# Optimization experiments

Measured on AMD Instinct MI355X. Metric: run time of the kernel, lower is better.

The kernel has to match this reference:

```python
import jax, jax.numpy as jnp
import numpy as np

NUM_HEADS = 8

def setup_inputs() -> dict:
    key = jax.random.key(0)
    ks = jax.random.split(key, 7)
    B, C, H, W = 8, 256, 32, 32
    scale = 1.0 / np.sqrt(C)
    return {
        "x": jax.random.normal(ks[0], (B, C, H, W), dtype=jnp.float32),
        "Wq": jax.random.normal(ks[1], (C, C), dtype=jnp.float32) * scale,
        "bq": jax.random.normal(ks[2], (C,), dtype=jnp.float32) * 0.01,
        "Wk": jax.random.normal(ks[3], (C, C), dtype=jnp.float32) * scale,
        "bk": jax.random.normal(ks[4], (C,), dtype=jnp.float32) * 0.01,
        "Wv": jax.random.normal(ks[5], (C, C), dtype=jnp.float32) * scale,
        "bv": jax.random.normal(ks[6], (C,), dtype=jnp.float32) * 0.01,
        "gamma": jnp.zeros((1,), dtype=jnp.float32),
    }

def reference(x, Wq, bq, Wk, bk, Wv, bv, gamma):
    B, C, H, W = x.shape
    nh = NUM_HEADS
    hd = C // nh
    N = H * W
    xf = x.reshape(B, C, N)  # flatten spatial dims; 1x1 conv == channel matmul

    def proj(Wt, bt):
        y = jnp.einsum('oc,bcn->bon', Wt, xf) + bt[None, :, None]
        return y.reshape(B, nh, hd, N)

    q = proj(Wq, bq)  # [B, h, d, N]
    k = proj(Wk, bk)
    v = proj(Wv, bv)

    # scores: q^T k over head_dim -> [B, h, N, N]
    scores = jnp.einsum('bhdn,bhdm->bhnm', q, k) / (hd ** 0.5)
    attn = jax.nn.softmax(scores, axis=-1)
    # out = attn @ v^T, arranged back to [B, h, d, N]
    out = jnp.einsum('bhnm,bhdm->bhdn', attn, v).reshape(B, C, H, W)
    return gamma * out + x
```

## Files before the change

kernel.cpp:

```cpp
#include <hip/hip_runtime.h>

typedef float f4 __attribute__((ext_vector_type(4)));
typedef __bf16 bf16x8 __attribute__((ext_vector_type(8)));
typedef unsigned short us4 __attribute__((ext_vector_type(4)));
typedef unsigned short us8 __attribute__((ext_vector_type(8)));
typedef unsigned int u2 __attribute__((ext_vector_type(2)));

#define NB 8
#define NC 256
#define NSP 1024
#define NH 8
#define HD 32
#define QSCALE_L2E 0.25506065038580317f

__device__ __forceinline__ unsigned short f2bf(float f) {
  unsigned u = __builtin_bit_cast(unsigned, f);
  u += 0x7FFFu + ((u >> 16) & 1u);
  return (unsigned short)(u >> 16);
}

__device__ __forceinline__ unsigned pkbf(float a, float b) {
  unsigned r;
  asm("v_cvt_pk_bf16_f32 %0, %1, %2" : "=v"(r) : "v"(a), "v"(b));
  return r;
}

__global__ __launch_bounds__(256) void prep_kernel(
    const float* __restrict__ x, const float* __restrict__ Wq,
    const float* __restrict__ Wk, const float* __restrict__ Wv,
    unsigned short* __restrict__ xT, unsigned short* __restrict__ wbf) {
  const int t = threadIdx.x;
  if (blockIdx.z == 8) {
    const int flat = (blockIdx.y * 16 + blockIdx.x) * 256 + t;
    const float* Ws[3] = {Wq, Wk, Wv};
#pragma unroll
    for (int p = 0; p < 3; ++p) {
      const f4 v = reinterpret_cast<const f4*>(Ws[p])[flat];
      us4 o;
#pragma unroll
      for (int j = 0; j < 4; ++j) o[j] = f2bf(v[j]);
      reinterpret_cast<us4*>(wbf + (size_t)p * 65536)[flat] = o;
    }
    return;
  }
  const int b = blockIdx.z;
  const int nt = blockIdx.x * 64, ct = blockIdx.y * 64;
  __shared__ float xs[64][72];
  const int cl = t >> 4, nl = (t & 15) * 4;
#pragma unroll
  for (int r = 0; r < 4; ++r) {
    const f4 v = *reinterpret_cast<const f4*>(
        &x[((size_t)(b * NC + ct + cl + r * 16)) * NSP + nt + nl]);
    *reinterpret_cast<f4*>(&xs[cl + r * 16][nl]) = v;
  }
  __syncthreads();
  const int n = t >> 2, cq = (t & 3) * 16;
  us8 o0, o1;
#pragma unroll
  for (int i = 0; i < 8; ++i) o0[i] = f2bf(xs[cq + i][n]);
#pragma unroll
  for (int i = 0; i < 8; ++i) o1[i] = f2bf(xs[cq + 8 + i][n]);
  const size_t base = ((size_t)(b * NSP + nt + n)) * NC + ct + cq;
  *reinterpret_cast<us8*>(&xT[base]) = o0;
  *reinterpret_cast<us8*>(&xT[base + 8]) = o1;
}

__global__ __launch_bounds__(256) void proj_qkv_kernel(
    const unsigned short* __restrict__ wbf, const float* __restrict__ bq,
    const float* __restrict__ bk, const float* __restrict__ bv,
    const unsigned short* __restrict__ xT, unsigned short* __restrict__ dq,
    unsigned short* __restrict__ dk, unsigned short* __restrict__ dv) {
  const int id = blockIdx.x;
  const int xcd = id & 7, rem = id >> 3;
  const int z = rem % 3;
  const int p = xcd + 8 * (rem / 3);
  const int ntile = (p & 15) * 64;
  const int b = p >> 4;

  const unsigned short* W = wbf + (size_t)z * 65536;
  const float* bias = (z == 0) ? bq : (z == 1) ? bk : bv;
  unsigned short* dst = (z == 0) ? dq : (z == 1) ? dk : dv;

  const int t = threadIdx.x, wid = t >> 6, lane = t & 63;
  const int lr = lane & 15, lg = lane >> 4;
  const int o0 = wid * 64;
  const size_t xbase = ((size_t)b * NSP + ntile) * NC;

  f4 acc[4][4] = {};
  for (int kk = 0; kk < NC; kk += 32) {
    bf16x8 wf[4], xf[4];
#pragma unroll
    for (int i = 0; i < 4; ++i)
      wf[i] = *reinterpret_cast<const bf16x8*>(
          &W[(size_t)(o0 + i * 16 + lr) * NC + kk + lg * 8]);
#pragma unroll
    for (int j = 0; j < 4; ++j)
      xf[j] = *reinterpret_cast<const bf16x8*>(
          &xT[xbase + (size_t)(j * 16 + lr) * NC + kk + lg * 8]);
    if (z != 2) {
#pragma unroll
      for (int i = 0; i < 4; ++i)
#pragma unroll
        for (int j = 0; j < 4; ++j)
          acc[i][j] = __builtin_amdgcn_mfma_f32_16x16x32_bf16(
              wf[i], xf[j], acc[i][j], 0, 0, 0);
    } else {
#pragma unroll
      for (int i = 0; i < 4; ++i)
#pragma unroll
        for (int j = 0; j < 4; ++j)
          acc[i][j] = __builtin_amdgcn_mfma_f32_16x16x32_bf16(
              xf[i], wf[j], acc[i][j], 0, 0, 0);
    }
  }

  if (z != 2) {
    const float scale = (z == 0) ? QSCALE_L2E : 1.0f;
#pragma unroll
    for (int i = 0; i < 4; ++i) {
      const int o = o0 + i * 16 + lg * 4;
      const f4 bvv = *reinterpret_cast<const f4*>(&bias[o]);
      const int h = o >> 5, d = o & 31;
#pragma unroll
      for (int j = 0; j < 4; ++j) {
        const int n = ntile + j * 16 + lr;
        us4 pk;
#pragma unroll
        for (int r = 0; r < 4; ++r) pk[r] = f2bf((acc[i][j][r] + bvv[r]) * scale);
        *reinterpret_cast<us4*>(
            &dst[(((size_t)b * NH + h) * NSP + n) * HD + d]) = pk;
      }
    }
  } else {
#pragma unroll
    for (int j = 0; j < 4; ++j) {
      const int o = o0 + j * 16 + lr;
      const float bo = bias[o];
      const int h = o >> 5, d = o & 31;
#pragma unroll
      for (int i = 0; i < 4; ++i) {
        const int n = ntile + i * 16 + lg * 4;
        us4 pk;
#pragma unroll
        for (int r = 0; r < 4; ++r) pk[r] = f2bf(acc[i][j][r] + bo);
        *reinterpret_cast<us4*>(
            &dst[(((size_t)b * NH + h) * HD + d) * NSP + n]) = pk;
      }
    }
  }
}

__global__ __launch_bounds__(256) void attn_kernel(
    const unsigned short* __restrict__ qs, const unsigned short* __restrict__ ks,
    const unsigned short* __restrict__ vt, const float* __restrict__ x,
    const float* __restrict__ gamma, float* __restrict__ out) {
  const int id = blockIdx.x;
  const int xcd = id & 7, slot = id >> 3;
  const int bh = xcd * 8 + (slot & 7);
  const int qt = slot >> 3;
  const int t = threadIdx.x, wid = t >> 6, lane = t & 63;
  const int lr = lane & 15, lg = lane >> 4;
  const int qbase = qt * 128 + wid * 32;

  __shared__ unsigned short plds[4][32][72];
  unsigned short* pw = &plds[wid][0][0];

  const size_t kvbase = (size_t)bh * (NSP * HD);
  bf16x8 qa[2];
#pragma unroll
  for (int qf = 0; qf < 2; ++qf)
    qa[qf] = *reinterpret_cast<const bf16x8*>(
        &qs[kvbase + (size_t)(qbase + qf * 16 + lr) * HD + lg * 8]);

  const unsigned short* kp = ks + kvbase;
  const unsigned short* vp = vt + kvbase;

  f4 acc[2][2] = {};
  float ls[2] = {0.f, 0.f};

  bf16x8 kb[4], vb[4];
#pragma unroll
  for (int kf = 0; kf < 4; ++kf)
    kb[kf] = *reinterpret_cast<const bf16x8*>(
        &kp[(size_t)(kf * 16 + lr) * HD + lg * 8]);
#pragma unroll
  for (int i = 0; i < 4; ++i) {
    const int sk = i >> 1, c = i & 1;
    vb[i] = *reinterpret_cast<const bf16x8*>(
        &vp[(size_t)(c * 16 + lr) * NSP + sk * 32 + lg * 8]);
  }

  for (int kt = 0; kt < NSP; kt += 64) {
    bf16x8 ck[4], cv[4];
#pragma unroll
    for (int i = 0; i < 4; ++i) { ck[i] = kb[i]; cv[i] = vb[i]; }
    const int nk = (kt + 64) & (NSP - 1);
#pragma unroll
    for (int kf = 0; kf < 4; ++kf)
      kb[kf] = *reinterpret_cast<const bf16x8*>(
          &kp[(size_t)(nk + kf * 16 + lr) * HD + lg * 8]);
#pragma unroll
    for (int i = 0; i < 4; ++i) {
      const int sk = i >> 1, c = i & 1;
      vb[i] = *reinterpret_cast<const bf16x8*>(
          &vp[(size_t)(c * 16 + lr) * NSP + nk + sk * 32 + lg * 8]);
    }

    const f4 z4 = {0.f, 0.f, 0.f, 0.f};
    f4 st[2][4];
#pragma unroll
    for (int qf = 0; qf < 2; ++qf)
#pragma unroll
      for (int kf = 0; kf < 4; ++kf)
        st[qf][kf] =
            __builtin_amdgcn_mfma_f32_16x16x32_bf16(ck[kf], qa[qf], z4, 0, 0, 0);

#pragma unroll
    for (int qf = 0; qf < 2; ++qf) {
      float lsum = 0.f;
#pragma unroll
      for (int kf = 0; kf < 4; ++kf) {
        f4 e;
#pragma unroll
        for (int r = 0; r < 4; ++r) e[r] = __builtin_exp2f(st[qf][kf][r]);
        lsum += (e[0] + e[1]) + (e[2] + e[3]);
        u2 wv = {pkbf(e[0], e[1]), pkbf(e[2], e[3])};
        *reinterpret_cast<u2*>(&pw[(qf * 16 + lr) * 72 + kf * 16 + lg * 4]) = wv;
      }
      ls[qf] += lsum;
    }

    bf16x8 pa[2][2];
#pragma unroll
    for (int sk = 0; sk < 2; ++sk)
#pragma unroll
      for (int qf = 0; qf < 2; ++qf)
        pa[sk][qf] = *reinterpret_cast<const bf16x8*>(
            &pw[(qf * 16 + lr) * 72 + sk * 32 + lg * 8]);

#pragma unroll
    for (int sk = 0; sk < 2; ++sk)
#pragma unroll
      for (int qf = 0; qf < 2; ++qf)
#pragma unroll
        for (int c = 0; c < 2; ++c)
          acc[qf][c] = __builtin_amdgcn_mfma_f32_16x16x32_bf16(
              pa[sk][qf], cv[sk * 2 + c], acc[qf][c], 0, 0, 0);
  }

#pragma unroll
  for (int qf = 0; qf < 2; ++qf) {
    ls[qf] += __shfl_xor(ls[qf], 16);
    ls[qf] += __shfl_xor(ls[qf], 32);
  }

  const int b = bh >> 3, h = bh & 7;
  const float g = gamma[0];
  const size_t ob = ((size_t)b * NC + h * HD) * NSP;

#pragma unroll
  for (int qf = 0; qf < 2; ++qf) {
    f4 li;
#pragma unroll
    for (int r = 0; r < 4; ++r) {
      const int src = (lg * 4 + r) * 4;
      li[r] = __builtin_amdgcn_rcpf(__builtin_bit_cast(
          float,
          __builtin_amdgcn_ds_bpermute(src, __builtin_bit_cast(int, ls[qf]))));
    }
#pragma unroll
    for (int c = 0; c < 2; ++c) {
      const size_t oa =
          ob + (size_t)(c * 16 + lr) * NSP + qbase + qf * 16 + lg * 4;
      const f4 xr = *reinterpret_cast<const f4*>(&x[oa]);
      f4 ov;
#pragma unroll
      for (int r = 0; r < 4; ++r) ov[r] = g * acc[qf][c][r] * li[r] + xr[r];
      *reinterpret_cast<f4*>(&out[oa]) = ov;
    }
  }
}

extern "C" void kernel_launch(void* const* d_in, const int* in_sizes, int n_in,
                              void* d_out, int out_size, void* d_ws,
                              size_t ws_size, hipStream_t stream) {
  const float* x = (const float*)d_in[0];
  const float* Wq = (const float*)d_in[1];
  const float* bq = (const float*)d_in[2];
  const float* Wk = (const float*)d_in[3];
  const float* bk = (const float*)d_in[4];
  const float* Wv = (const float*)d_in[5];
  const float* bv = (const float*)d_in[6];
  const float* gamma = (const float*)d_in[7];
  float* out = (float*)d_out;

  unsigned short* qs = (unsigned short*)d_ws;
  unsigned short* ks = qs + (size_t)2097152;
  unsigned short* vt = ks + (size_t)2097152;
  unsigned short* wbf = vt + (size_t)2097152;
  unsigned short* xT = wbf + (size_t)3 * 65536;

  prep_kernel<<<dim3(16, 4, 9), 256, 0, stream>>>(x, Wq, Wk, Wv, xT, wbf);
  proj_qkv_kernel<<<dim3(384), 256, 0, stream>>>(wbf, bq, bk, bv, xT, qs, ks,
                                                 vt);
  attn_kernel<<<dim3(512), 256, 0, stream>>>(qs, ks, vt, x, gamma, out);
}
```

Before: 126.8 us.

## Fuse x transpose/bf16 conversion into QKV projection via shared memory

Result: faster. 122.1 us (-3.7%).

```diff
diff --git a/kernel.cpp b/kernel.cpp
--- a/kernel.cpp
+++ b/kernel.cpp
@@ -3,7 +3,6 @@
 typedef float f4 __attribute__((ext_vector_type(4)));
 typedef __bf16 bf16x8 __attribute__((ext_vector_type(8)));
 typedef unsigned short us4 __attribute__((ext_vector_type(4)));
-typedef unsigned short us8 __attribute__((ext_vector_type(8)));
 typedef unsigned int u2 __attribute__((ext_vector_type(2)));
 
 #define NB 8
@@ -25,126 +24,115 @@
   return r;
 }
 
-__global__ __launch_bounds__(256) void prep_kernel(
-    const float* __restrict__ x, const float* __restrict__ Wq,
-    const float* __restrict__ Wk, const float* __restrict__ Wv,
-    unsigned short* __restrict__ xT, unsigned short* __restrict__ wbf) {
-  const int t = threadIdx.x;
-  if (blockIdx.z == 8) {
-    const int flat = (blockIdx.y * 16 + blockIdx.x) * 256 + t;
-    const float* Ws[3] = {Wq, Wk, Wv};
-#pragma unroll
-    for (int p = 0; p < 3; ++p) {
-      const f4 v = reinterpret_cast<const f4*>(Ws[p])[flat];
-      us4 o;
-#pragma unroll
-      for (int j = 0; j < 4; ++j) o[j] = f2bf(v[j]);
-      reinterpret_cast<us4*>(wbf + (size_t)p * 65536)[flat] = o;
-    }
-    return;
-  }
-  const int b = blockIdx.z;
-  const int nt = blockIdx.x * 64, ct = blockIdx.y * 64;
-  __shared__ float xs[64][72];
-  const int cl = t >> 4, nl = (t & 15) * 4;
-#pragma unroll
-  for (int r = 0; r < 4; ++r) {
-    const f4 v = *reinterpret_cast<const f4*>(
-        &x[((size_t)(b * NC + ct + cl + r * 16)) * NSP + nt + nl]);
-    *reinterpret_cast<f4*>(&xs[cl + r * 16][nl]) = v;
-  }
-  __syncthreads();
-  const int n = t >> 2, cq = (t & 3) * 16;
-  us8 o0, o1;
-#pragma unroll
-  for (int i = 0; i < 8; ++i) o0[i] = f2bf(xs[cq + i][n]);
-#pragma unroll
-  for (int i = 0; i < 8; ++i) o1[i] = f2bf(xs[cq + 8 + i][n]);
-  const size_t base = ((size_t)(b * NSP + nt + n)) * NC + ct + cq;
-  *reinterpret_cast<us8*>(&xT[base]) = o0;
-  *reinterpret_cast<us8*>(&xT[base + 8]) = o1;
+__global__ __launch_bounds__(256) void prep_w_kernel(
+    const float* __restrict__ Wq, const float* __restrict__ Wk,
+    const float* __restrict__ Wv, unsigned short* __restrict__ wbf) {
+  const int id = blockIdx.x;
+  const int z = id >> 6;
+  const int flat = (id & 63) * 256 + threadIdx.x;
+  const float* W = (z == 0) ? Wq : (z == 1) ? Wk : Wv;
+  const f4 v = reinterpret_cast<const f4*>(W)[flat];
+  us4 o;
+#pragma unroll
+  for (int j = 0; j < 4; ++j) o[j] = f2bf(v[j]);
+  reinterpret_cast<us4*>(wbf + (size_t)z * 65536)[flat] = o;
 }
 
 __global__ __launch_bounds__(256) void proj_qkv_kernel(
     const unsigned short* __restrict__ wbf, const float* __restrict__ bq,
     const float* __restrict__ bk, const float* __restrict__ bv,
-    const unsigned short* __restrict__ xT, unsigned short* __restrict__ dq,
+    const float* __restrict__ x, unsigned short* __restrict__ dq,
     unsigned short* __restrict__ dk, unsigned short* __restrict__ dv) {
   const int id = blockIdx.x;
-  const int xcd = id & 7, rem = id >> 3;
-  const int z = rem % 3;
-  const int p = xcd + 8 * (rem / 3);
-  const int ntile = (p & 15) * 64;
-  const int b = p >> 4;
-
-  const unsigned short* W = wbf + (size_t)z * 65536;
-  const float* bias = (z == 0) ? bq : (z == 1) ? bk : bv;
-  unsigned short* dst = (z == 0) ? dq : (z == 1) ? dk : dv;
+  const int xcd = id & 7, slot = id >> 3;
+  const int pair = xcd * 32 + (slot >> 1);
+  const int og = slot & 1;
+  const int b = pair >> 5, nt = pair & 31;
 
   const int t = threadIdx.x, wid = t >> 6, lane = t & 63;
   const int lr = lane & 15, lg = lane >> 4;
-  const int o0 = wid * 64;
-  const size_t xbase = ((size_t)b * NSP + ntile) * NC;
-
-  f4 acc[4][4] = {};
-  for (int kk = 0; kk < NC; kk += 32) {
-    bf16x8 wf[4], xf[4];
-#pragma unroll
-    for (int i = 0; i < 4; ++i)
-      wf[i] = *reinterpret_cast<const bf16x8*>(
-          &W[(size_t)(o0 + i * 16 + lr) * NC + kk + lg * 8]);
-#pragma unroll
-    for (int j = 0; j < 4; ++j)
-      xf[j] = *reinterpret_cast<const bf16x8*>(
-          &xT[xbase + (size_t)(j * 16 + lr) * NC + kk + lg * 8]);
+
+  __shared__ unsigned short xls[32][264];
+
+  {
+    const int n0 = (t & 7) * 4, c0 = t >> 3;
+    const float* xp = x + (size_t)b * NC * NSP + (size_t)nt * 32;
+#pragma unroll
+    for (int cc = 0; cc < NC; cc += 32) {
+      const f4 v =
+          *reinterpret_cast<const f4*>(&xp[(size_t)(cc + c0) * NSP + n0]);
+#pragma unroll
+      for (int j = 0; j < 4; ++j) xls[n0 + j][cc + c0] = f2bf(v[j]);
+    }
+  }
+  __syncthreads();
+
+  const int o0 = og * 128 + wid * 32;
+  const int h = og * 4 + wid;
+
+  for (int z = 0; z < 3; ++z) {
+    const unsigned short* W = wbf + (size_t)z * 65536;
+    f4 acc[2][2] = {};
+    for (int kk = 0; kk < NC; kk += 32) {
+      bf16x8 wf[2], xf[2];
+#pragma unroll
+      for (int i = 0; i < 2; ++i)
+        wf[i] = *reinterpret_cast<const bf16x8*>(
+            &W[(size_t)(o0 + i * 16 + lr) * NC + kk + lg * 8]);
+#pragma unroll
+      for (int j = 0; j < 2; ++j)
+        xf[j] = *reinterpret_cast<const bf16x8*>(
+            &xls[j * 16 + lr][kk + lg * 8]);
+      if (z != 2) {
+#pragma unroll
+        for (int i = 0; i < 2; ++i)
+#pragma unroll
+          for (int j = 0; j < 2; ++j)
+            acc[i][j] = __builtin_amdgcn_mfma_f32_16x16x32_bf16(
+                wf[i], xf[j], acc[i][j], 0, 0, 0);
+      } else {
+#pragma unroll
+        for (int i = 0; i < 2; ++i)
+#pragma unroll
+          for (int j = 0; j < 2; ++j)
+            acc[i][j] = __builtin_amdgcn_mfma_f32_16x16x32_bf16(
+                xf[i], wf[j], acc[i][j], 0, 0, 0);
+      }
+    }
+
+    const float* bias = (z == 0) ? bq : (z == 1) ? bk : bv;
+    unsigned short* dst = (z == 0) ? dq : (z == 1) ? dk : dv;
     if (z != 2) {
-#pragma unroll
-      for (int i = 0; i < 4; ++i)
-#pragma unroll
-        for (int j = 0; j < 4; ++j)
-          acc[i][j] = __builtin_amdgcn_mfma_f32_16x16x32_bf16(
-              wf[i], xf[j], acc[i][j], 0, 0, 0);
+      const float scale = (z == 0) ? QSCALE_L2E : 1.0f;
+#pragma unroll
+      for (int i = 0; i < 2; ++i) {
+        const int d0 = i * 16 + lg * 4;
+        const f4 bv4 = *reinterpret_cast<const f4*>(&bias[o0 + d0]);
+#pragma unroll
+        for (int j = 0; j < 2; ++j) {
+          const int n = nt * 32 + j * 16 + lr;
+          us4 pk;
+#pragma unroll
+          for (int r = 0; r < 4; ++r)
+            pk[r] = f2bf((acc[i][j][r] + bv4[r]) * scale);
+          *reinterpret_cast<us4*>(
+              &dst[(((size_t)b * NH + h) * NSP + n) * HD + d0]) = pk;
+        }
+      }
     } else {
 #pragma unroll
-      for (int i = 0; i < 4; ++i)
-#pragma unroll
-        for (int j = 0; j < 4; ++j)
-          acc[i][j] = __builtin_amdgcn_mfma_f32_16x16x32_bf16(
-              xf[i], wf[j], acc[i][j], 0, 0, 0);
-    }
-  }
-
-  if (z != 2) {
-    const float scale = (z == 0) ? QSCALE_L2E : 1.0f;
-#pragma unroll
-    for (int i = 0; i < 4; ++i) {
-      const int o = o0 + i * 16 + lg * 4;
-      const f4 bvv = *reinterpret_cast<const f4*>(&bias[o]);
-      const int h = o >> 5, d = o & 31;
-#pragma unroll
-      for (int j = 0; j < 4; ++j) {
-        const int n = ntile + j * 16 + lr;
-        us4 pk;
-#pragma unroll
-        for (int r = 0; r < 4; ++r) pk[r] = f2bf((acc[i][j][r] + bvv[r]) * scale);
-        *reinterpret_cast<us4*>(
-            &dst[(((size_t)b * NH + h) * NSP + n) * HD + d]) = pk;
-      }
-    }
-  } else {
-#pragma unroll
-    for (int j = 0; j < 4; ++j) {
-      const int o = o0 + j * 16 + lr;
-      const float bo = bias[o];
-      const int h = o >> 5, d = o & 31;
-#pragma unroll
-      for (int i = 0; i < 4; ++i) {
-        const int n = ntile + i * 16 + lg * 4;
-        us4 pk;
-#pragma unroll
-        for (int r = 0; r < 4; ++r) pk[r] = f2bf(acc[i][j][r] + bo);
-        *reinterpret_cast<us4*>(
-            &dst[(((size_t)b * NH + h) * HD + d) * NSP + n]) = pk;
+      for (int j = 0; j < 2; ++j) {
+        const int d = j * 16 + lr;
+        const float bo = bias[o0 + d];
+#pragma unroll
+        for (int i = 0; i < 2; ++i) {
+          const int n = nt * 32 + i * 16 + lg * 4;
+          us4 pk;
+#pragma unroll
+          for (int r = 0; r < 4; ++r) pk[r] = f2bf(acc[i][j][r] + bo);
+          *reinterpret_cast<us4*>(
+              &dst[(((size_t)b * NH + h) * HD + d) * NSP + n]) = pk;
+        }
       }
     }
   }
@@ -298,10 +286,9 @@
   unsigned short* ks = qs + (size_t)2097152;
   unsigned short* vt = ks + (size_t)2097152;
   unsigned short* wbf = vt + (size_t)2097152;
-  unsigned short* xT = wbf + (size_t)3 * 65536;
-
-  prep_kernel<<<dim3(16, 4, 9), 256, 0, stream>>>(x, Wq, Wk, Wv, xT, wbf);
-  proj_qkv_kernel<<<dim3(384), 256, 0, stream>>>(wbf, bq, bk, bv, xT, qs, ks,
+
+  prep_w_kernel<<<dim3(192), 256, 0, stream>>>(Wq, Wk, Wv, wbf);
+  proj_qkv_kernel<<<dim3(512), 256, 0, stream>>>(wbf, bq, bk, bv, x, qs, ks,
                                                  vt);
   attn_kernel<<<dim3(512), 256, 0, stream>>>(qs, ks, vt, x, gamma, out);
 }
```
